# Performance work log

Measured on AMD Instinct MI355X. Metric: run time of the kernel, lower is better.

Reference implementation:

```python
import jax, jax.numpy as jnp
import numpy as np

D_MODEL = 1024
H = 16
D_K = D_MODEL // H


def setup_inputs() -> dict:
    key = jax.random.key(0)
    ks = jax.random.split(key, 12)
    B, S = 2, 2048
    q = jax.random.normal(ks[0], (B, S, D_MODEL), dtype=jnp.float32)
    k = jax.random.normal(ks[1], (B, S, D_MODEL), dtype=jnp.float32)
    v = jax.random.normal(ks[2], (B, S, D_MODEL), dtype=jnp.float32)
    mask = jax.random.randint(ks[3], (1, 1, S, S), 0, 2, dtype=jnp.int32)
    sc = 1.0 / np.sqrt(D_MODEL)
    wq = jax.random.uniform(ks[4], (D_MODEL, D_MODEL), jnp.float32, -sc, sc)
    bq = jax.random.uniform(ks[5], (D_MODEL,), jnp.float32, -sc, sc)
    wk = jax.random.uniform(ks[6], (D_MODEL, D_MODEL), jnp.float32, -sc, sc)
    bk = jax.random.uniform(ks[7], (D_MODEL,), jnp.float32, -sc, sc)
    wv = jax.random.uniform(ks[8], (D_MODEL, D_MODEL), jnp.float32, -sc, sc)
    bv = jax.random.uniform(ks[9], (D_MODEL,), jnp.float32, -sc, sc)
    wo = jax.random.uniform(ks[10], (D_MODEL, D_MODEL), jnp.float32, -sc, sc)
    bo = jax.random.uniform(ks[11], (D_MODEL,), jnp.float32, -sc, sc)
    return {"q": q, "k": k, "v": v, "mask": mask,
            "wq": wq, "bq": bq, "wk": wk, "bk": bk,
            "wv": wv, "bv": bv, "wo": wo, "bo": bo}


def reference(q, k, v, mask, wq, bq, wk, bk, wv, bv, wo, bo):
    B, S, _ = q.shape
    # linear projections (torch Linear: x @ W.T + b)
    query = q @ wq.T + bq
    key = k @ wk.T + bk
    value = v @ wv.T + bv
    # [B, S, D] -> [B, H, S, d_k]
    query = query.reshape(B, S, H, D_K).transpose(0, 2, 1, 3)
    key = key.reshape(B, S, H, D_K).transpose(0, 2, 1, 3)
    value = value.reshape(B, S, H, D_K).transpose(0, 2, 1, 3)
    scores = jnp.einsum('bhqd,bhkd->bhqk', query, key) / jnp.sqrt(
        jnp.asarray(D_K, query.dtype))
    # NOTE: source uses `-1 ** 9` which is -1 in Python, not -1e9 (soft mask)
    scores = jnp.where(mask == 0, jnp.asarray(-1.0, scores.dtype), scores)
    attn = jax.nn.softmax(scores, axis=-1)
    # source calls dropout(attn) but discards the result -> no-op
    x = jnp.einsum('bhqk,bhkd->bhqd', attn, value)
    x = x.transpose(0, 2, 1, 3).reshape(B, S, H * D_K)
    return x @ wo.T + bo
```

## Files before the change

kernel.cpp:

```cpp
#include <hip/hip_runtime.h>
#include <hip/hip_bf16.h>

#define D_MODEL 1024
#define NH 16
#define DK 64
#define S_LEN 2048
#define BATCH 2
#define M_ROWS (BATCH * S_LEN)

typedef float    floatx4 __attribute__((ext_vector_type(4)));
typedef _Float16 half8   __attribute__((ext_vector_type(8)));
typedef _Float16 half4v  __attribute__((ext_vector_type(4)));

#define LOG2E 1.4426950408889634f

__device__ __forceinline__ half8 ldh8(const _Float16* p) {
    return __builtin_bit_cast(half8, *(const uint4*)p);
}
__device__ __forceinline__ void gld16(const void* g, void* l) {
    __builtin_amdgcn_global_load_lds(
        (const __attribute__((address_space(1))) void*)g,
        (__attribute__((address_space(3))) void*)l, 16, 0, 0);
}
__device__ __forceinline__ float dpp_swap1(float x) {
    return __builtin_bit_cast(float,
        __builtin_amdgcn_mov_dpp(__builtin_bit_cast(int, x), 0xB1, 0xF, 0xF, false));
}

__global__ __launch_bounds__(256)
void cast_h(const float* __restrict__ s0, const float* __restrict__ s1,
            const float* __restrict__ s2, const float* __restrict__ s3,
            _Float16* __restrict__ out, int R) {
    const int z = blockIdx.y;
    const float* src = (z == 0) ? s0 : (z == 1) ? s1 : (z == 2) ? s2 : s3;
    const size_t idx = ((size_t)blockIdx.x * 256 + threadIdx.x) * 4;
    float4 v = *(const float4*)&src[idx];
    half4v h = {(_Float16)v.x, (_Float16)v.y, (_Float16)v.z, (_Float16)v.w};
    *(half4v*)&out[(size_t)z * R * 1024 + idx] = h;
}

template <int OUTMODE>
__global__ __launch_bounds__(256)
void gemm_f16(const _Float16* __restrict__ Abase, const _Float16* __restrict__ Wbase,
              const float* __restrict__ b0, const float* __restrict__ b1,
              const float* __restrict__ b2, void* __restrict__ Obase) {
    __shared__ __align__(16) _Float16 As[128 * 64];
    __shared__ __align__(16) _Float16 Ws[128 * 64];
    const int tid = threadIdx.x;
    const int w = tid >> 6, lane = tid & 63;
    const int l15 = lane & 15, q4 = lane >> 4;
    const int z = (OUTMODE == 1) ? blockIdx.z : 0;
    const int m0 = blockIdx.y * 128, n0 = blockIdx.x * 128;
    const int wm = w >> 1, wn = w & 1;

    const _Float16* A = Abase + (size_t)z * M_ROWS * 1024;
    const _Float16* W = Wbase + (size_t)z * 1024 * 1024;
    const float* bias = (OUTMODE == 1) ? ((z == 0) ? b0 : (z == 1) ? b1 : b2) : b0;

    int srow[4], sseg[4];
#pragma unroll
    for (int i = 0; i < 4; i++) {
        const int slot = i * 256 + tid;
        srow[i] = slot >> 3;
        sseg[i] = ((slot & 7) ^ (srow[i] & 7)) * 8;
    }

    int aoff[4][2], woff[4][2];
#pragma unroll
    for (int r = 0; r < 4; r++) {
        const int ar = wm * 64 + r * 16 + l15;
        const int wr = wn * 64 + r * 16 + l15;
#pragma unroll
        for (int kc = 0; kc < 2; kc++) {
            aoff[r][kc] = (ar * 8 + ((kc * 4 + q4) ^ (ar & 7))) * 8;
            woff[r][kc] = (wr * 8 + ((kc * 4 + q4) ^ (wr & 7))) * 8;
        }
    }

    floatx4 acc[4][4];
#pragma unroll
    for (int r = 0; r < 4; r++)
#pragma unroll
        for (int c = 0; c < 4; c++) acc[r][c] = (floatx4){0.f, 0.f, 0.f, 0.f};

    for (int k0 = 0; k0 < 1024; k0 += 64) {
#pragma unroll
        for (int i = 0; i < 4; i++) {
            const int lb = (i * 256 + w * 64) * 8;
            gld16(&A[(size_t)(m0 + srow[i]) * 1024 + k0 + sseg[i]], &As[lb]);
            gld16(&W[(size_t)(n0 + srow[i]) * 1024 + k0 + sseg[i]], &Ws[lb]);
        }
        __syncthreads();

        half8 af[4][2], wf[4][2];
#pragma unroll
        for (int r = 0; r < 4; r++)
#pragma unroll
            for (int kc = 0; kc < 2; kc++) {
                af[r][kc] = ldh8(&As[aoff[r][kc]]);
                wf[r][kc] = ldh8(&Ws[woff[r][kc]]);
            }
#pragma unroll
        for (int kc = 0; kc < 2; kc++)
#pragma unroll
            for (int r = 0; r < 4; r++)
#pragma unroll
                for (int c = 0; c < 4; c++)
                    acc[r][c] = __builtin_amdgcn_mfma_f32_16x16x32_f16(
                        af[r][kc], wf[c][kc], acc[r][c], 0, 0, 0);
        __syncthreads();
    }

#pragma unroll
    for (int r = 0; r < 4; r++)
#pragma unroll
        for (int c = 0; c < 4; c++)
#pragma unroll
            for (int reg = 0; reg < 4; reg++) {
                const int m = m0 + wm * 64 + r * 16 + q4 * 4 + reg;
                const int n = n0 + wn * 64 + c * 16 + l15;
                float val = acc[r][c][reg] + bias[n];
                if (OUTMODE == 0) {
                    ((float*)Obase)[(size_t)m * 1024 + n] = val;
                } else {
                    if (z == 0) val *= 0.125f * LOG2E;
                    const int b = m >> 11, s = m & 2047;
                    const int h = n >> 6, d = n & 63;
                    _Float16* Oz = (_Float16*)Obase + (size_t)z * M_ROWS * 1024;
                    Oz[(((size_t)(b * 16 + h) * S_LEN + s) << 6) + d] = (_Float16)val;
                }
            }
}

__global__ __launch_bounds__(256)
void vt_trans(const short* __restrict__ Vh, short* __restrict__ Vt) {
    __shared__ __align__(16) short T[64][80];
    const int bh = blockIdx.y;
    const int s0 = blockIdx.x * 64;
    const int t = threadIdx.x;
#pragma unroll
    for (int i = 0; i < 2; i++) {
        const int p = t + i * 256, r = p >> 3, c8 = (p & 7) * 8;
        uint4 raw = *(const uint4*)&Vh[((size_t)bh * S_LEN + s0 + r) * 64 + c8];
        const short* sv = (const short*)&raw;
#pragma unroll
        for (int j = 0; j < 8; j++) T[c8 + j][r] = sv[j];
    }
    __syncthreads();
#pragma unroll
    for (int i = 0; i < 2; i++) {
        const int p = t + i * 256, d = p >> 3, seg = (p & 7) * 8;
        *(uint4*)&Vt[((size_t)bh * DK + d) * S_LEN + s0 + seg] =
            *(const uint4*)&T[d][seg];
    }
}

__global__ __launch_bounds__(256)
void mask_pack(const int* __restrict__ mask, unsigned long long* __restrict__ mb) {
    const int gw = blockIdx.x * 4 + (threadIdx.x >> 6);
    const int lane = threadIdx.x & 63;
    const int row = gw >> 5, wid = gw & 31;
    const int mv = mask[(size_t)row * S_LEN + wid * 64 + lane];
    unsigned long long bal = __ballot(mv != 0);
    if (lane == 0) mb[gw] = bal;
}

__global__ __launch_bounds__(256)
void attn_mfma(const _Float16* __restrict__ Qh, const _Float16* __restrict__ Kh,
               const _Float16* __restrict__ Vt, const unsigned long long* __restrict__ mb,
               _Float16* __restrict__ Xh) {
    __shared__ __align__(16) _Float16 Ks[64 * 64];
    __shared__ __align__(16) _Float16 Vs[64 * 64];
    __shared__ __align__(16) _Float16 Ps[4][32 * 72];

    const int tid = threadIdx.x;
    const int w = tid >> 6, lane = tid & 63;
    const int l15 = lane & 15, q4 = lane >> 4;
    const int bh = blockIdx.y, b = bh >> 4, h = bh & 15;
    const int qb = blockIdx.x * 128 + w * 32;

    const _Float16* Qg = Qh + ((size_t)bh * S_LEN + qb) * DK;
    const _Float16* Kg = Kh + (size_t)bh * S_LEN * DK;
    const _Float16* Vg = Vt + (size_t)bh * DK * S_LEN;

    half8 Aq[2][2];
#pragma unroll
    for (int qs = 0; qs < 2; qs++)
#pragma unroll
        for (int ch = 0; ch < 2; ch++)
            Aq[qs][ch] = ldh8(&Qg[(qs * 16 + l15) * DK + ch * 32 + q4 * 8]);

    int grow[2], gseg[2];
#pragma unroll
    for (int i = 0; i < 2; i++) {
        const int slot = i * 256 + tid;
        grow[i] = slot >> 3;
        gseg[i] = ((slot & 7) ^ (grow[i] & 7)) * 8;
    }

    int foff[4][2];
#pragma unroll
    for (int t4 = 0; t4 < 4; t4++)
#pragma unroll
        for (int ch = 0; ch < 2; ch++)
            foff[t4][ch] = (t4 * 16 + l15) * 64 + (((ch * 4 + q4) ^ (l15 & 7)) * 8);

    int mrow[2][4];
#pragma unroll
    for (int qs = 0; qs < 2; qs++)
#pragma unroll
        for (int reg = 0; reg < 4; reg++)
            mrow[qs][reg] = (qb + qs * 16 + q4 * 4 + reg) * (S_LEN / 64);

    floatx4 O[2][4];
#pragma unroll
    for (int qs = 0; qs < 2; qs++)
#pragma unroll
        for (int nt = 0; nt < 4; nt++) O[qs][nt] = (floatx4){0.f, 0.f, 0.f, 0.f};
    float lsum[2][4] = {{0.f, 0.f, 0.f, 0.f}, {0.f, 0.f, 0.f, 0.f}};

    const bool evenlane = ((lane & 1) == 0);

    for (int j0 = 0; j0 < S_LEN; j0 += 64) {
#pragma unroll
        for (int i = 0; i < 2; i++) {
            const int lb = (i * 256 + w * 64) * 8;
            gld16(&Kg[(size_t)(j0 + grow[i]) * DK + gseg[i]], &Ks[lb]);
            gld16(&Vg[(size_t)grow[i] * S_LEN + j0 + gseg[i]], &Vs[lb]);
        }
        const int jw = j0 >> 6;
        unsigned long long mw[2][4];
#pragma unroll
        for (int qs = 0; qs < 2; qs++)
#pragma unroll
            for (int reg = 0; reg < 4; reg++)
                mw[qs][reg] = mb[mrow[qs][reg] + jw];
        __syncthreads();

        half8 Kf[4][2];
#pragma unroll
        for (int jt = 0; jt < 4; jt++)
#pragma unroll
            for (int ch = 0; ch < 2; ch++)
                Kf[jt][ch] = ldh8(&Ks[foff[jt][ch]]);

#pragma unroll
        for (int qs = 0; qs < 2; qs++) {
            floatx4 Sf[4];
#pragma unroll
            for (int jt = 0; jt < 4; jt++) {
                floatx4 c = (floatx4){0.f, 0.f, 0.f, 0.f};
                c = __builtin_amdgcn_mfma_f32_16x16x32_f16(Aq[qs][0], Kf[jt][0], c, 0, 0, 0);
                c = __builtin_amdgcn_mfma_f32_16x16x32_f16(Aq[qs][1], Kf[jt][1], c, 0, 0, 0);
                Sf[jt] = c;
            }
#pragma unroll
            for (int reg = 0; reg < 4; reg++) {
                const unsigned long long m = mw[qs][reg];
#pragma unroll
                for (int jt = 0; jt < 4; jt++) {
                    float s = Sf[jt][reg];
                    s = ((m >> (jt * 16 + l15)) & 1ull) ? s : -LOG2E;
                    const float p = __builtin_amdgcn_exp2f(s);
                    lsum[qs][reg] += p;
                    const float po = dpp_swap1(p);
                    if (evenlane) {
                        *(unsigned*)&Ps[w][(qs * 16 + q4 * 4 + reg) * 72 +
                                           jt * 16 + l15] =
                            __builtin_bit_cast(unsigned,
                                __builtin_amdgcn_cvt_pkrtz(p, po));
                    }
                }
            }
        }

#pragma unroll
        for (int qs = 0; qs < 2; qs++) {
            half8 Ap[2];
#pragma unroll
            for (int ch = 0; ch < 2; ch++)
                Ap[ch] = ldh8(&Ps[w][(qs * 16 + l15) * 72 + ch * 32 + q4 * 8]);
#pragma unroll
            for (int nt = 0; nt < 4; nt++) {
                O[qs][nt] = __builtin_amdgcn_mfma_f32_16x16x32_f16(
                    Ap[0], ldh8(&Vs[foff[nt][0]]), O[qs][nt], 0, 0, 0);
                O[qs][nt] = __builtin_amdgcn_mfma_f32_16x16x32_f16(
                    Ap[1], ldh8(&Vs[foff[nt][1]]), O[qs][nt], 0, 0, 0);
            }
        }
        __syncthreads();
    }

#pragma unroll
    for (int qs = 0; qs < 2; qs++)
#pragma unroll
        for (int reg = 0; reg < 4; reg++) {
#pragma unroll
            for (int off = 1; off < 16; off <<= 1)
                lsum[qs][reg] += __shfl_xor(lsum[qs][reg], off, 64);
        }
#pragma unroll
    for (int qs = 0; qs < 2; qs++)
#pragma unroll
        for (int reg = 0; reg < 4; reg++) {
            const float inv = 1.0f / lsum[qs][reg];
            const int srow = qb + qs * 16 + q4 * 4 + reg;
            _Float16* Xrow = Xh + (size_t)(b * S_LEN + srow) * 1024 + h * DK;
#pragma unroll
            for (int nt = 0; nt < 4; nt++)
                Xrow[nt * 16 + l15] = (_Float16)(O[qs][nt][reg] * inv);
        }
}

extern "C" void kernel_launch(void* const* d_in, const int* in_sizes, int n_in,
                              void* d_out, int out_size, void* d_ws, size_t ws_size,
                              hipStream_t stream) {
    const float* q  = (const float*)d_in[0];
    const float* k  = (const float*)d_in[1];
    const float* v  = (const float*)d_in[2];
    const int* mask = (const int*)d_in[3];
    const float* wq = (const float*)d_in[4];
    const float* bq = (const float*)d_in[5];
    const float* wk = (const float*)d_in[6];
    const float* bk = (const float*)d_in[7];
    const float* wv = (const float*)d_in[8];
    const float* bv = (const float*)d_in[9];
    const float* wo = (const float*)d_in[10];
    const float* bo = (const float*)d_in[11];
    float* out = (float*)d_out;

    char* ws = (char*)d_ws;
    const size_t MB = 1u << 20;
    _Float16* Wh   = (_Float16*)ws;
    _Float16* Ah   = (_Float16*)(ws + 8 * MB);
    _Float16* QKVh = (_Float16*)(ws + 32 * MB);
    _Float16* Vt   = (_Float16*)(ws + 56 * MB);
    unsigned long long* mb = (unsigned long long*)(ws + 64 * MB);
    _Float16* Xh   = Ah;

    cast_h<<<dim3(1024, 4), 256, 0, stream>>>(wq, wk, wv, wo, Wh, 1024);
    cast_h<<<dim3(4096, 3), 256, 0, stream>>>(q, k, v, nullptr, Ah, M_ROWS);

    gemm_f16<1><<<dim3(8, 32, 3), 256, 0, stream>>>(Ah, Wh, bq, bk, bv, QKVh);

    vt_trans<<<dim3(32, 32), 256, 0, stream>>>(
        (const short*)(QKVh + (size_t)2 * M_ROWS * 1024), (short*)Vt);
    mask_pack<<<S_LEN * (S_LEN / 64) / 4, 256, 0, stream>>>(mask, mb);

    attn_mfma<<<dim3(16, 32), 256, 0, stream>>>(QKVh, QKVh + (size_t)M_ROWS * 1024,
                                                Vt, mb, Xh);

    gemm_f16<0><<<dim3(8, 32, 1), 256, 0, stream>>>(Xh, Wh + (size_t)3 * 1024 * 1024,
                                                    bo, bo, bo, out);
}
```

Baseline: 292.6 us.

## Split attention key range across two wave groups and compute row sums via MFMA

```diff
diff --git a/kernel.cpp b/kernel.cpp
--- a/kernel.cpp
+++ b/kernel.cpp
@@ -13,6 +13,7 @@
 typedef _Float16 half4v  __attribute__((ext_vector_type(4)));
 
 #define LOG2E 1.4426950408889634f
+#define EXPM1 0.36787944117144233f
 
 __device__ __forceinline__ half8 ldh8(const _Float16* p) {
     return __builtin_bit_cast(half8, *(const uint4*)p);
@@ -165,23 +166,26 @@
     if (lane == 0) mb[gw] = bal;
 }
 
-__global__ __launch_bounds__(256)
+__global__ __launch_bounds__(512, 4)
 void attn_mfma(const _Float16* __restrict__ Qh, const _Float16* __restrict__ Kh,
                const _Float16* __restrict__ Vt, const unsigned long long* __restrict__ mb,
                _Float16* __restrict__ Xh) {
-    __shared__ __align__(16) _Float16 Ks[64 * 64];
-    __shared__ __align__(16) _Float16 Vs[64 * 64];
-    __shared__ __align__(16) _Float16 Ps[4][32 * 72];
+    __shared__ __align__(16) _Float16 Ks[2][64 * 64];
+    __shared__ __align__(16) _Float16 Vs[2][64 * 64];
+    __shared__ __align__(16) _Float16 Ps[8][32 * 72];
 
     const int tid = threadIdx.x;
     const int w = tid >> 6, lane = tid & 63;
+    const int z = w >> 2, w4 = w & 3;
+    const int t255 = tid & 255;
     const int l15 = lane & 15, q4 = lane >> 4;
     const int bh = blockIdx.y, b = bh >> 4, h = bh & 15;
-    const int qb = blockIdx.x * 128 + w * 32;
+    const int qb = blockIdx.x * 128 + w4 * 32;
+    const int kbase = z * 1024;
 
     const _Float16* Qg = Qh + ((size_t)bh * S_LEN + qb) * DK;
-    const _Float16* Kg = Kh + (size_t)bh * S_LEN * DK;
-    const _Float16* Vg = Vt + (size_t)bh * DK * S_LEN;
+    const _Float16* Kg = Kh + ((size_t)bh * S_LEN + kbase) * DK;
+    const _Float16* Vg = Vt + (size_t)bh * DK * S_LEN + kbase;
 
     half8 Aq[2][2];
 #pragma unroll
@@ -193,7 +197,7 @@
     int grow[2], gseg[2];
 #pragma unroll
     for (int i = 0; i < 2; i++) {
-        const int slot = i * 256 + tid;
+        const int slot = i * 256 + t255;
         grow[i] = slot >> 3;
         gseg[i] = ((slot & 7) ^ (grow[i] & 7)) * 8;
     }
@@ -210,23 +214,29 @@
     for (int qs = 0; qs < 2; qs++)
 #pragma unroll
         for (int reg = 0; reg < 4; reg++)
-            mrow[qs][reg] = (qb + qs * 16 + q4 * 4 + reg) * (S_LEN / 64);
+            mrow[qs][reg] = (qb + qs * 16 + q4 * 4 + reg) * (S_LEN / 64) + z * 16;
 
     floatx4 O[2][4];
 #pragma unroll
     for (int qs = 0; qs < 2; qs++)
 #pragma unroll
         for (int nt = 0; nt < 4; nt++) O[qs][nt] = (floatx4){0.f, 0.f, 0.f, 0.f};
-    float lsum[2][4] = {{0.f, 0.f, 0.f, 0.f}, {0.f, 0.f, 0.f, 0.f}};
+    floatx4 lacc[2];
+    lacc[0] = (floatx4){0.f, 0.f, 0.f, 0.f};
+    lacc[1] = (floatx4){0.f, 0.f, 0.f, 0.f};
+
+    half8 onesB;
+#pragma unroll
+    for (int i = 0; i < 8; i++) onesB[i] = (_Float16)1.0f;
 
     const bool evenlane = ((lane & 1) == 0);
 
-    for (int j0 = 0; j0 < S_LEN; j0 += 64) {
+    for (int j0 = 0; j0 < 1024; j0 += 64) {
 #pragma unroll
         for (int i = 0; i < 2; i++) {
-            const int lb = (i * 256 + w * 64) * 8;
-            gld16(&Kg[(size_t)(j0 + grow[i]) * DK + gseg[i]], &Ks[lb]);
-            gld16(&Vg[(size_t)grow[i] * S_LEN + j0 + gseg[i]], &Vs[lb]);
+            const int lb = (i * 256 + w4 * 64) * 8;
+            gld16(&Kg[(size_t)(j0 + grow[i]) * DK + gseg[i]], &Ks[z][lb]);
+            gld16(&Vg[(size_t)grow[i] * S_LEN + j0 + gseg[i]], &Vs[z][lb]);
         }
         const int jw = j0 >> 6;
         unsigned long long mw[2][4];
@@ -242,7 +252,7 @@
         for (int jt = 0; jt < 4; jt++)
 #pragma unroll
             for (int ch = 0; ch < 2; ch++)
-                Kf[jt][ch] = ldh8(&Ks[foff[jt][ch]]);
+                Kf[jt][ch] = ldh8(&Ks[z][foff[jt][ch]]);
 
 #pragma unroll
         for (int qs = 0; qs < 2; qs++) {
@@ -257,12 +267,13 @@
 #pragma unroll
             for (int reg = 0; reg < 4; reg++) {
                 const unsigned long long m = mw[qs][reg];
+                const unsigned tt0 = (unsigned)m >> l15;
+                const unsigned tt1 = (unsigned)(m >> 32) >> l15;
 #pragma unroll
                 for (int jt = 0; jt < 4; jt++) {
-                    float s = Sf[jt][reg];
-                    s = ((m >> (jt * 16 + l15)) & 1ull) ? s : -LOG2E;
-                    const float p = __builtin_amdgcn_exp2f(s);
-                    lsum[qs][reg] += p;
+                    float p = __builtin_amdgcn_exp2f(Sf[jt][reg]);
+                    const unsigned sel = (jt < 2 ? tt0 : tt1) & (1u << ((jt & 1) * 16));
+                    p = sel ? p : EXPM1;
                     const float po = dpp_swap1(p);
                     if (evenlane) {
                         *(unsigned*)&Ps[w][(qs * 16 + q4 * 4 + reg) * 72 +
@@ -280,36 +291,48 @@
 #pragma unroll
             for (int ch = 0; ch < 2; ch++)
                 Ap[ch] = ldh8(&Ps[w][(qs * 16 + l15) * 72 + ch * 32 + q4 * 8]);
+            lacc[qs] = __builtin_amdgcn_mfma_f32_16x16x32_f16(Ap[0], onesB, lacc[qs], 0, 0, 0);
+            lacc[qs] = __builtin_amdgcn_mfma_f32_16x16x32_f16(Ap[1], onesB, lacc[qs], 0, 0, 0);
 #pragma unroll
             for (int nt = 0; nt < 4; nt++) {
                 O[qs][nt] = __builtin_amdgcn_mfma_f32_16x16x32_f16(
-                    Ap[0], ldh8(&Vs[foff[nt][0]]), O[qs][nt], 0, 0, 0);
+                    Ap[0], ldh8(&Vs[z][foff[nt][0]]), O[qs][nt], 0, 0, 0);
                 O[qs][nt] = __builtin_amdgcn_mfma_f32_16x16x32_f16(
-                    Ap[1], ldh8(&Vs[foff[nt][1]]), O[qs][nt], 0, 0, 0);
+                    Ap[1], ldh8(&Vs[z][foff[nt][1]]), O[qs][nt], 0, 0, 0);
             }
         }
         __syncthreads();
     }
 
-#pragma unroll
-    for (int qs = 0; qs < 2; qs++)
-#pragma unroll
-        for (int reg = 0; reg < 4; reg++) {
-#pragma unroll
-            for (int off = 1; off < 16; off <<= 1)
-                lsum[qs][reg] += __shfl_xor(lsum[qs][reg], off, 64);
-        }
-#pragma unroll
-    for (int qs = 0; qs < 2; qs++)
-#pragma unroll
-        for (int reg = 0; reg < 4; reg++) {
-            const float inv = 1.0f / lsum[qs][reg];
-            const int srow = qb + qs * 16 + q4 * 4 + reg;
-            _Float16* Xrow = Xh + (size_t)(b * S_LEN + srow) * 1024 + h * DK;
-#pragma unroll
-            for (int nt = 0; nt < 4; nt++)
-                Xrow[nt * 16 + l15] = (_Float16)(O[qs][nt][reg] * inv);
-        }
+    float* Obuf = (float*)&Ps[0][0];
+    if (z == 1) {
+#pragma unroll
+        for (int qs = 0; qs < 2; qs++)
+#pragma unroll
+            for (int reg = 0; reg < 4; reg++) {
+                const int rl = w4 * 32 + qs * 16 + q4 * 4 + reg;
+#pragma unroll
+                for (int nt = 0; nt < 4; nt++)
+                    Obuf[rl * 65 + nt * 16 + l15] = O[qs][nt][reg];
+                if (l15 == 0) Obuf[rl * 65 + 64] = lacc[qs][reg];
+            }
+    }
+    __syncthreads();
+    if (z == 0) {
+#pragma unroll
+        for (int qs = 0; qs < 2; qs++)
+#pragma unroll
+            for (int reg = 0; reg < 4; reg++) {
+                const int rl = w4 * 32 + qs * 16 + q4 * 4 + reg;
+                const float inv = 1.0f / (lacc[qs][reg] + Obuf[rl * 65 + 64]);
+                const int srow = qb + qs * 16 + q4 * 4 + reg;
+                _Float16* Xrow = Xh + (size_t)(b * S_LEN + srow) * 1024 + h * DK;
+#pragma unroll
+                for (int nt = 0; nt < 4; nt++)
+                    Xrow[nt * 16 + l15] =
+                        (_Float16)((O[qs][nt][reg] + Obuf[rl * 65 + nt * 16 + l15]) * inv);
+            }
+    }
 }
 
 extern "C" void kernel_launch(void* const* d_in, const int* in_sizes, int n_in,
@@ -347,7 +370,7 @@
         (const short*)(QKVh + (size_t)2 * M_ROWS * 1024), (short*)Vt);
     mask_pack<<<S_LEN * (S_LEN / 64) / 4, 256, 0, stream>>>(mask, mb);
 
-    attn_mfma<<<dim3(16, 32), 256, 0, stream>>>(QKVh, QKVh + (size_t)M_ROWS * 1024,
+    attn_mfma<<<dim3(16, 32), 512, 0, stream>>>(QKVh, QKVh + (size_t)M_ROWS * 1024,
                                                 Vt, mb, Xh);
 
     gemm_f16<0><<<dim3(8, 32, 1), 256, 0, stream>>>(Xh, Wh + (size_t)3 * 1024 * 1024,
```

Result: slower. 337.0 us (+15.2%).
